# Kernel tuning notes

Measured on AMD Instinct MI355X. Metric: run time of the kernel, lower is better.

Reference implementation:

```python
import jax, jax.numpy as jnp
import numpy as np


def setup_inputs() -> dict:
    key = jax.random.key(0)
    k1, k2, k3 = jax.random.split(key, 3)
    B, H, S, D = 2, 8, 4096, 64
    queries = jax.random.normal(k1, (B, H, S, D), dtype=jnp.float32)
    keys = jax.random.normal(k2, (B, H, S, D), dtype=jnp.float32)
    values = jax.random.normal(k3, (B, H, S, D), dtype=jnp.float32)
    mask = jnp.zeros((1, 1, S, S), dtype=jnp.float32)
    return {"queries": queries, "keys": keys, "values": values, "d_k": D, "mask": mask}


def reference(queries, keys, values, d_k, mask):
    # scores: [B, H, Sq, Sk]
    scale = 1.0 / jnp.sqrt(jnp.asarray(d_k, dtype=queries.dtype))
    scores = jnp.einsum("bhqd,bhkd->bhqk", queries, keys) * scale
    scores = scores + (-1e9) * mask  # additive mask, broadcasts over B, H
    weights = jax.nn.softmax(scores, axis=-1)
    return jnp.einsum("bhqk,bhkd->bhqd", weights, values)
```

## Files before the change

kernel.cpp:

```cpp
#include <hip/hip_runtime.h>

#define S_LEN 4096
#define DHEAD 64
#define BQ    128
#define BK    64
#define NT    (S_LEN / BK)
#define KPAD  72

typedef __fp16   pk16x2 __attribute__((ext_vector_type(2)));
typedef _Float16 half4v __attribute__((ext_vector_type(4)));
typedef _Float16 half8  __attribute__((ext_vector_type(8)));
typedef float    f32x4  __attribute__((ext_vector_type(4)));

__global__ void mask_flag_kernel(const float4* __restrict__ mask, int* __restrict__ flag) {
    const long stride = 2048L * 256;
    long i = (long)blockIdx.x * 256 + threadIdx.x;
    int nz = 0;
    #pragma unroll
    for (int it = 0; it < 8; ++it) {
        float4 a = mask[i + it * stride];
        nz |= (a.x != 0.f) | (a.y != 0.f) | (a.z != 0.f) | (a.w != 0.f);
    }
    if (__any(nz)) {
        if ((threadIdx.x & 63) == 0) atomicOr(flag, 1);
    }
}

__global__ __launch_bounds__(256, 2) void attn_kernel(
    const float* __restrict__ Q, const float* __restrict__ K,
    const float* __restrict__ V, const int* __restrict__ dk,
    const float* __restrict__ mask, const int* __restrict__ maskflag,
    float* __restrict__ O)
{
    const int qt   = blockIdx.x;
    const int bh   = blockIdx.y;
    const int tid  = threadIdx.x;
    const int wave = tid >> 6;
    const int lane = tid & 63;
    const int l15  = lane & 15;
    const int quad = lane >> 4;

    const long base = (long)bh * S_LEN * DHEAD;
    const float* Qh = Q + base;
    const float* Kh = K + base;
    const float* Vh = V + base;
    float*       Oh = O + base;

    const int q0 = qt * BQ + wave * 32;
    const float csq  = rsqrtf((float)dk[0]) * 1.44269504088896f;
    const float mfac = -1e9f * 1.44269504088896f;
    const bool use_mask = (maskflag[0] != 0);

    __shared__ __align__(16) _Float16 Kt[2][BK][KPAD];
    __shared__ __align__(16) _Float16 Vt[2][DHEAD * KPAD];
    __shared__ __align__(16) _Float16 Pw[4][32][KPAD];

    half8 qf[2][2];
    #pragma unroll
    for (int f = 0; f < 2; ++f) {
        #pragma unroll
        for (int kc = 0; kc < 2; ++kc) {
            const float4* src = (const float4*)(Qh + (long)(q0 + f*16 + l15) * DHEAD + kc*32 + quad*8);
            float4 a = src[0], b = src[1];
            union { pk16x2 p[4]; half8 h; } u;
            u.p[0] = __builtin_amdgcn_cvt_pkrtz(a.x*csq, a.y*csq);
            u.p[1] = __builtin_amdgcn_cvt_pkrtz(a.z*csq, a.w*csq);
            u.p[2] = __builtin_amdgcn_cvt_pkrtz(b.x*csq, b.y*csq);
            u.p[3] = __builtin_amdgcn_cvt_pkrtz(b.z*csq, b.w*csq);
            qf[f][kc] = u.h;
        }
    }

    const int kr  = tid >> 2;
    const int ks  = tid & 3;
    const int vrp = tid >> 3;
    const int vdq = tid & 7;
    const float* Kb = Kh + (long)kr * DHEAD + ks * 16;
    const float* Vb = Vh + (long)(2 * vrp) * DHEAD + vdq * 8;
    const int vcol = (((vrp >> 2) ^ vdq) << 3) + ((2 * vrp) & 7);
    const int vd0  = vdq * 8;

    float4 kf[4], vf[4];
    auto load_tile = [&](int kt) {
        const float4* kp  = (const float4*)(Kb + (long)kt * BK * DHEAD);
        kf[0] = kp[0]; kf[1] = kp[1]; kf[2] = kp[2]; kf[3] = kp[3];
        const float4* vp0 = (const float4*)(Vb + (long)kt * BK * DHEAD);
        const float4* vp1 = (const float4*)(Vb + (long)kt * BK * DHEAD + DHEAD);
        vf[0] = vp0[0]; vf[1] = vp0[1]; vf[2] = vp1[0]; vf[3] = vp1[1];
    };
    auto store_tile = [&](int b) {
        union { pk16x2 p[4]; half8 h; } u0, u1;
        u0.p[0] = __builtin_amdgcn_cvt_pkrtz(kf[0].x, kf[0].y);
        u0.p[1] = __builtin_amdgcn_cvt_pkrtz(kf[0].z, kf[0].w);
        u0.p[2] = __builtin_amdgcn_cvt_pkrtz(kf[1].x, kf[1].y);
        u0.p[3] = __builtin_amdgcn_cvt_pkrtz(kf[1].z, kf[1].w);
        u1.p[0] = __builtin_amdgcn_cvt_pkrtz(kf[2].x, kf[2].y);
        u1.p[1] = __builtin_amdgcn_cvt_pkrtz(kf[2].z, kf[2].w);
        u1.p[2] = __builtin_amdgcn_cvt_pkrtz(kf[3].x, kf[3].y);
        u1.p[3] = __builtin_amdgcn_cvt_pkrtz(kf[3].z, kf[3].w);
        *(half8*)&Kt[b][kr][ks*16]     = u0.h;
        *(half8*)&Kt[b][kr][ks*16 + 8] = u1.h;
        _Float16* vt = &Vt[b][0];
        *(pk16x2*)&vt[(vd0+0)*KPAD + vcol] = __builtin_amdgcn_cvt_pkrtz(vf[0].x, vf[2].x);
        *(pk16x2*)&vt[(vd0+1)*KPAD + vcol] = __builtin_amdgcn_cvt_pkrtz(vf[0].y, vf[2].y);
        *(pk16x2*)&vt[(vd0+2)*KPAD + vcol] = __builtin_amdgcn_cvt_pkrtz(vf[0].z, vf[2].z);
        *(pk16x2*)&vt[(vd0+3)*KPAD + vcol] = __builtin_amdgcn_cvt_pkrtz(vf[0].w, vf[2].w);
        *(pk16x2*)&vt[(vd0+4)*KPAD + vcol] = __builtin_amdgcn_cvt_pkrtz(vf[1].x, vf[3].x);
        *(pk16x2*)&vt[(vd0+5)*KPAD + vcol] = __builtin_amdgcn_cvt_pkrtz(vf[1].y, vf[3].y);
        *(pk16x2*)&vt[(vd0+6)*KPAD + vcol] = __builtin_amdgcn_cvt_pkrtz(vf[1].z, vf[3].z);
        *(pk16x2*)&vt[(vd0+7)*KPAD + vcol] = __builtin_amdgcn_cvt_pkrtz(vf[1].w, vf[3].w);
    };

    f32x4 o[2][4];
    #pragma unroll
    for (int f = 0; f < 2; ++f)
        #pragma unroll
        for (int dt = 0; dt < 4; ++dt) o[f][dt] = (f32x4){0.f, 0.f, 0.f, 0.f};
    float m_i[2] = {-INFINITY, -INFINITY};
    float l_i[2] = {0.0f, 0.0f};

    load_tile(0);
    store_tile(0);
    __syncthreads();

    for (int kt = 0; kt < NT; ++kt) {
        const int b = kt & 1;
        if (kt + 1 < NT) load_tile(kt + 1);

        f32x4 st[2][4];
        #pragma unroll
        for (int f = 0; f < 2; ++f)
            #pragma unroll
            for (int nt = 0; nt < 4; ++nt) st[f][nt] = (f32x4){0.f,0.f,0.f,0.f};
        #pragma unroll
        for (int nt = 0; nt < 4; ++nt) {
            #pragma unroll
            for (int kc = 0; kc < 2; ++kc) {
                half8 af = *(const half8*)&Kt[b][nt*16 + l15][kc*32 + quad*8];
                st[0][nt] = __builtin_amdgcn_mfma_f32_16x16x32_f16(af, qf[0][kc], st[0][nt], 0, 0, 0);
                st[1][nt] = __builtin_amdgcn_mfma_f32_16x16x32_f16(af, qf[1][kc], st[1][nt], 0, 0, 0);
            }
        }

        if (use_mask) {
            #pragma unroll
            for (int f = 0; f < 2; ++f) {
                const long mrow = (long)(q0 + f*16 + l15) * S_LEN + kt*BK;
                #pragma unroll
                for (int nt = 0; nt < 4; ++nt)
                    #pragma unroll
                    for (int r = 0; r < 4; ++r)
                        st[f][nt][r] += mfac * mask[mrow + nt*16 + quad*4 + r];
            }
        }

        float alpha[2];
        #pragma unroll
        for (int f = 0; f < 2; ++f) {
            float mx = fmaxf(fmaxf(fmaxf(st[f][0][0], st[f][0][1]), fmaxf(st[f][0][2], st[f][0][3])),
                             fmaxf(fmaxf(st[f][1][0], st[f][1][1]), fmaxf(st[f][1][2], st[f][1][3])));
            float mx2 = fmaxf(fmaxf(fmaxf(st[f][2][0], st[f][2][1]), fmaxf(st[f][2][2], st[f][2][3])),
                              fmaxf(fmaxf(st[f][3][0], st[f][3][1]), fmaxf(st[f][3][2], st[f][3][3])));
            mx = fmaxf(mx, mx2);
            mx = fmaxf(mx, __shfl_xor(mx, 16, 64));
            mx = fmaxf(mx, __shfl_xor(mx, 32, 64));
            float mnew = fmaxf(m_i[f], mx);
            float rsum = 0.0f;
            #pragma unroll
            for (int nt = 0; nt < 4; ++nt) {
                #pragma unroll
                for (int r = 0; r < 4; ++r) {
                    float p = __builtin_amdgcn_exp2f(st[f][nt][r] - mnew);
                    st[f][nt][r] = p;
                    rsum += p;
                }
            }
            rsum += __shfl_xor(rsum, 16, 64);
            rsum += __shfl_xor(rsum, 32, 64);
            alpha[f] = __builtin_amdgcn_exp2f(m_i[f] - mnew);
            l_i[f] = alpha[f] * l_i[f] + rsum;
            m_i[f] = mnew;
        }

        #pragma unroll
        for (int f = 0; f < 2; ++f)
            #pragma unroll
            for (int r = 0; r < 4; ++r) {
                float a_r = __shfl(alpha[f], quad*4 + r, 64);
                #pragma unroll
                for (int dt = 0; dt < 4; ++dt) o[f][dt][r] *= a_r;
            }

        #pragma unroll
        for (int f = 0; f < 2; ++f)
            #pragma unroll
            for (int nt = 0; nt < 4; ++nt) {
                union { pk16x2 p[2]; half4v h; } up;
                up.p[0] = __builtin_amdgcn_cvt_pkrtz(st[f][nt][0], st[f][nt][1]);
                up.p[1] = __builtin_amdgcn_cvt_pkrtz(st[f][nt][2], st[f][nt][3]);
                *(half4v*)&Pw[wave][f*16 + l15][nt*16 + quad*4] = up.h;
            }

        #pragma unroll
        for (int kc2 = 0; kc2 < 2; ++kc2) {
            half8 pa0 = *(const half8*)&Pw[wave][l15][kc2*32 + quad*8];
            half8 pa1 = *(const half8*)&Pw[wave][16 + l15][kc2*32 + quad*8];
            #pragma unroll
            for (int dt = 0; dt < 4; ++dt) {
                const int row = dt*16 + l15;
                const int pb  = (4*kc2 + quad) ^ (row >> 3);
                half8 vb = *(const half8*)&Vt[b][row*KPAD + pb*8];
                o[0][dt] = __builtin_amdgcn_mfma_f32_16x16x32_f16(pa0, vb, o[0][dt], 0, 0, 0);
                o[1][dt] = __builtin_amdgcn_mfma_f32_16x16x32_f16(pa1, vb, o[1][dt], 0, 0, 0);
            }
        }

        if (kt + 1 < NT) {
            store_tile((kt + 1) & 1);
            __syncthreads();
        }
    }

    #pragma unroll
    for (int f = 0; f < 2; ++f) {
        #pragma unroll
        for (int r = 0; r < 4; ++r) {
            float lq = __shfl(l_i[f], quad*4 + r, 64);
            float linv = __builtin_amdgcn_rcpf(lq);
            const long row = (long)(q0 + f*16 + quad*4 + r) * DHEAD;
            #pragma unroll
            for (int dt = 0; dt < 4; ++dt)
                Oh[row + dt*16 + l15] = o[f][dt][r] * linv;
        }
    }
}

extern "C" void kernel_launch(void* const* d_in, const int* in_sizes, int n_in,
                              void* d_out, int out_size, void* d_ws, size_t ws_size,
                              hipStream_t stream) {
    const float* Q    = (const float*)d_in[0];
    const float* K    = (const float*)d_in[1];
    const float* V    = (const float*)d_in[2];
    const int*   dk   = (const int*)d_in[3];
    const float* mask = (const float*)d_in[4];
    float* out = (float*)d_out;
    int* flag = (int*)d_ws;

    (void)hipMemsetAsync(flag, 0, sizeof(int), stream);
    mask_flag_kernel<<<2048, 256, 0, stream>>>((const float4*)mask, flag);

    dim3 grid(S_LEN / BQ, 16);
    attn_kernel<<<grid, 256, 0, stream>>>(Q, K, V, dk, mask, flag, out);
}
```

Measured before the change: 255.5 us.

## Pre-convert K/V to swizzled fp16 tiles and stream them via global_load_lds

Adds a prepass kernel that converts K and V to fp16 once per call, transposing V and writing XOR-swizzled 64x64 tiles into workspace. The same kernel also folds in the mask nonzero scan. The attention kernel then double-buffers these tiles into LDS with direct global-to-LDS loads, which avoids per-block fp32 loads and conversions repeated across the 32 query tiles. The cost is an extra pass over K/V plus a workspace dependency, and the old path is kept as a fallback when the workspace is too small.

```diff
diff --git a/kernel.cpp b/kernel.cpp
--- a/kernel.cpp
+++ b/kernel.cpp
@@ -6,12 +6,21 @@
 #define BK    64
 #define NT    (S_LEN / BK)
 #define KPAD  72
+#define NBH   16
+#define TILE_HALFS (BK * DHEAD)
+#define WS_KV_HALFS ((size_t)NBH * NT * TILE_HALFS)
 
 typedef __fp16   pk16x2 __attribute__((ext_vector_type(2)));
 typedef _Float16 half4v __attribute__((ext_vector_type(4)));
 typedef _Float16 half8  __attribute__((ext_vector_type(8)));
 typedef float    f32x4  __attribute__((ext_vector_type(4)));
 
+__device__ __forceinline__ void gl_lds16(const _Float16* g, _Float16* l) {
+    __builtin_amdgcn_global_load_lds(
+        (const __attribute__((address_space(1))) unsigned int*)g,
+        (__attribute__((address_space(3))) unsigned int*)l, 16, 0, 0);
+}
+
 __global__ void mask_flag_kernel(const float4* __restrict__ mask, int* __restrict__ flag) {
     const long stride = 2048L * 256;
     long i = (long)blockIdx.x * 256 + threadIdx.x;
@@ -26,7 +35,252 @@
     }
 }
 
-__global__ __launch_bounds__(256, 2) void attn_kernel(
+__global__ void conv_kernel(const float* __restrict__ Kg, const float* __restrict__ Vg,
+                            const float* __restrict__ mask,
+                            _Float16* __restrict__ wsK, _Float16* __restrict__ wsV,
+                            int* __restrict__ flag) {
+    const int tid  = threadIdx.x;
+    const int tile = blockIdx.x;
+    __shared__ __align__(16) _Float16 T[64][64];
+
+    if (blockIdx.y == 0) {
+        const float* Ksrc = Kg + (long)tile * TILE_HALFS;
+        _Float16*    dst  = wsK + (long)tile * TILE_HALFS;
+        #pragma unroll
+        for (int it = 0; it < 2; ++it) {
+            int m = tid + it * 256;
+            int r = m >> 3, c = m & 7;
+            const float4* s4 = (const float4*)(Ksrc + r * DHEAD + ((c ^ (r & 7)) << 3));
+            float4 a = s4[0], b = s4[1];
+            union { pk16x2 p[4]; half8 h; } u;
+            u.p[0] = __builtin_amdgcn_cvt_pkrtz(a.x, a.y);
+            u.p[1] = __builtin_amdgcn_cvt_pkrtz(a.z, a.w);
+            u.p[2] = __builtin_amdgcn_cvt_pkrtz(b.x, b.y);
+            u.p[3] = __builtin_amdgcn_cvt_pkrtz(b.z, b.w);
+            *(half8*)(dst + m * 8) = u.h;
+        }
+    } else if (blockIdx.y == 1) {
+        const float* Vsrc = Vg + (long)tile * TILE_HALFS;
+        const int r  = tid >> 2;
+        const int d0 = (tid & 3) << 4;
+        const float4* s4 = (const float4*)(Vsrc + r * DHEAD + d0);
+        float vv[16];
+        *(float4*)&vv[0]  = s4[0];
+        *(float4*)&vv[4]  = s4[1];
+        *(float4*)&vv[8]  = s4[2];
+        *(float4*)&vv[12] = s4[3];
+        #pragma unroll
+        for (int j = 0; j < 16; j += 2) {
+            pk16x2 p = __builtin_amdgcn_cvt_pkrtz(vv[j], vv[j + 1]);
+            T[d0 + j][r]     = *((_Float16*)&p);
+            T[d0 + j + 1][r] = *((_Float16*)&p + 1);
+        }
+        __syncthreads();
+        _Float16* dst = wsV + (long)tile * TILE_HALFS;
+        #pragma unroll
+        for (int it = 0; it < 2; ++it) {
+            int m = tid + it * 256;
+            int d = m >> 3, c = m & 7;
+            *(half8*)(dst + m * 8) = *(const half8*)&T[d][(c ^ (d & 7)) << 3];
+        }
+    } else {
+        const float4* m4 = (const float4*)mask;
+        const long stride = 1024L * 256;
+        long i = (long)blockIdx.x * 256 + tid;
+        int nz = 0;
+        #pragma unroll
+        for (int it = 0; it < 16; ++it) {
+            float4 a = m4[i + it * stride];
+            nz |= (a.x != 0.f) | (a.y != 0.f) | (a.z != 0.f) | (a.w != 0.f);
+        }
+        if (__any(nz)) {
+            if ((tid & 63) == 0) atomicOr(flag, 1);
+        }
+    }
+}
+
+__global__ __launch_bounds__(256, 2) void attn_ws_kernel(
+    const float* __restrict__ Q, const _Float16* __restrict__ KW,
+    const _Float16* __restrict__ VW, const int* __restrict__ dk,
+    const float* __restrict__ mask, const int* __restrict__ maskflag,
+    float* __restrict__ O)
+{
+    const int qt   = blockIdx.x;
+    const int bh   = blockIdx.y;
+    const int tid  = threadIdx.x;
+    const int wave = tid >> 6;
+    const int lane = tid & 63;
+    const int l15  = lane & 15;
+    const int quad = lane >> 4;
+    const int sw   = (l15 & 7) << 3;
+    const int rq8  = quad << 3;
+
+    const long base = (long)bh * S_LEN * DHEAD;
+    const float* Qh = Q + base;
+    float*       Oh = O + base;
+    const _Float16* gk = KW + (long)bh * (NT * TILE_HALFS);
+    const _Float16* gv = VW + (long)bh * (NT * TILE_HALFS);
+
+    const int q0 = qt * BQ + wave * 32;
+    const float csq  = rsqrtf((float)dk[0]) * 1.44269504088896f;
+    const float mfac = -1e9f * 1.44269504088896f;
+    const bool use_mask = (maskflag[0] != 0);
+
+    __shared__ __align__(16) _Float16 KT[2][TILE_HALFS];
+    __shared__ __align__(16) _Float16 VT[2][TILE_HALFS];
+    __shared__ __align__(16) _Float16 Pw[4][32][KPAD];
+
+    half8 qf[2][2];
+    #pragma unroll
+    for (int f = 0; f < 2; ++f) {
+        #pragma unroll
+        for (int kc = 0; kc < 2; ++kc) {
+            const float4* src = (const float4*)(Qh + (long)(q0 + f*16 + l15) * DHEAD + kc*32 + rq8);
+            float4 a = src[0], b = src[1];
+            union { pk16x2 p[4]; half8 h; } u;
+            u.p[0] = __builtin_amdgcn_cvt_pkrtz(a.x*csq, a.y*csq);
+            u.p[1] = __builtin_amdgcn_cvt_pkrtz(a.z*csq, a.w*csq);
+            u.p[2] = __builtin_amdgcn_cvt_pkrtz(b.x*csq, b.y*csq);
+            u.p[3] = __builtin_amdgcn_cvt_pkrtz(b.z*csq, b.w*csq);
+            qf[f][kc] = u.h;
+        }
+    }
+
+    auto stage = [&](int kt, int b) {
+        const _Float16* k8 = gk + (long)kt * TILE_HALFS + tid * 8;
+        const _Float16* v8 = gv + (long)kt * TILE_HALFS + tid * 8;
+        gl_lds16(k8,        &KT[b][tid * 8]);
+        gl_lds16(k8 + 2048, &KT[b][2048 + tid * 8]);
+        gl_lds16(v8,        &VT[b][tid * 8]);
+        gl_lds16(v8 + 2048, &VT[b][2048 + tid * 8]);
+    };
+
+    f32x4 o[2][4];
+    #pragma unroll
+    for (int f = 0; f < 2; ++f)
+        #pragma unroll
+        for (int dt = 0; dt < 4; ++dt) o[f][dt] = (f32x4){0.f, 0.f, 0.f, 0.f};
+    float m_i[2] = {-INFINITY, -INFINITY};
+    float l_i[2] = {0.0f, 0.0f};
+
+    stage(0, 0);
+    __syncthreads();
+
+    for (int kt = 0; kt < NT; ++kt) {
+        const int b = kt & 1;
+        if (kt + 1 < NT) stage(kt + 1, b ^ 1);
+
+        f32x4 st[2][4];
+        #pragma unroll
+        for (int f = 0; f < 2; ++f)
+            #pragma unroll
+            for (int nt = 0; nt < 4; ++nt) st[f][nt] = (f32x4){0.f,0.f,0.f,0.f};
+        __builtin_amdgcn_s_setprio(1);
+        #pragma unroll
+        for (int nt = 0; nt < 4; ++nt) {
+            const int rb = (nt << 10) + (l15 << 6);
+            #pragma unroll
+            for (int kc = 0; kc < 2; ++kc) {
+                half8 af = *(const half8*)&KT[b][rb + ((kc*32 + rq8) ^ sw)];
+                st[0][nt] = __builtin_amdgcn_mfma_f32_16x16x32_f16(af, qf[0][kc], st[0][nt], 0, 0, 0);
+                st[1][nt] = __builtin_amdgcn_mfma_f32_16x16x32_f16(af, qf[1][kc], st[1][nt], 0, 0, 0);
+            }
+        }
+        __builtin_amdgcn_s_setprio(0);
+
+        if (use_mask) {
+            #pragma unroll
+            for (int f = 0; f < 2; ++f) {
+                const long mrow = (long)(q0 + f*16 + l15) * S_LEN + kt*BK;
+                #pragma unroll
+                for (int nt = 0; nt < 4; ++nt)
+                    #pragma unroll
+                    for (int r = 0; r < 4; ++r)
+                        st[f][nt][r] += mfac * mask[mrow + nt*16 + quad*4 + r];
+            }
+        }
+
+        #pragma unroll
+        for (int f = 0; f < 2; ++f) {
+            float mx = fmaxf(fmaxf(fmaxf(st[f][0][0], st[f][0][1]), fmaxf(st[f][0][2], st[f][0][3])),
+                             fmaxf(fmaxf(st[f][1][0], st[f][1][1]), fmaxf(st[f][1][2], st[f][1][3])));
+            float mx2 = fmaxf(fmaxf(fmaxf(st[f][2][0], st[f][2][1]), fmaxf(st[f][2][2], st[f][2][3])),
+                              fmaxf(fmaxf(st[f][3][0], st[f][3][1]), fmaxf(st[f][3][2], st[f][3][3])));
+            mx = fmaxf(mx, mx2);
+            mx = fmaxf(mx, __shfl_xor(mx, 16, 64));
+            mx = fmaxf(mx, __shfl_xor(mx, 32, 64));
+            const bool need = __any(mx > m_i[f]);
+            const float mnew = need ? fmaxf(m_i[f], mx) : m_i[f];
+            float rsum = 0.0f;
+            #pragma unroll
+            for (int nt = 0; nt < 4; ++nt) {
+                #pragma unroll
+                for (int r = 0; r < 4; ++r) {
+                    float p = __builtin_amdgcn_exp2f(st[f][nt][r] - mnew);
+                    st[f][nt][r] = p;
+                    rsum += p;
+                }
+            }
+            rsum += __shfl_xor(rsum, 16, 64);
+            rsum += __shfl_xor(rsum, 32, 64);
+            if (need) {
+                const float alpha = __builtin_amdgcn_exp2f(m_i[f] - mnew);
+                #pragma unroll
+                for (int r = 0; r < 4; ++r) {
+                    float a_r = __shfl(alpha, quad*4 + r, 64);
+                    #pragma unroll
+                    for (int dt = 0; dt < 4; ++dt) o[f][dt][r] *= a_r;
+                }
+                l_i[f] = alpha * l_i[f] + rsum;
+                m_i[f] = mnew;
+            } else {
+                l_i[f] += rsum;
+            }
+        }
+
+        #pragma unroll
+        for (int f = 0; f < 2; ++f)
+            #pragma unroll
+            for (int nt = 0; nt < 4; ++nt) {
+                union { pk16x2 p[2]; half4v h; } up;
+                up.p[0] = __builtin_amdgcn_cvt_pkrtz(st[f][nt][0], st[f][nt][1]);
+                up.p[1] = __builtin_amdgcn_cvt_pkrtz(st[f][nt][2], st[f][nt][3]);
+                *(half4v*)&Pw[wave][f*16 + l15][nt*16 + quad*4] = up.h;
+            }
+
+        __builtin_amdgcn_s_setprio(1);
+        #pragma unroll
+        for (int kc2 = 0; kc2 < 2; ++kc2) {
+            half8 pa0 = *(const half8*)&Pw[wave][l15][kc2*32 + rq8];
+            half8 pa1 = *(const half8*)&Pw[wave][16 + l15][kc2*32 + rq8];
+            #pragma unroll
+            for (int dt = 0; dt < 4; ++dt) {
+                const int db = (dt << 10) + (l15 << 6);
+                half8 vb = *(const half8*)&VT[b][db + ((kc2*32 + rq8) ^ sw)];
+                o[0][dt] = __builtin_amdgcn_mfma_f32_16x16x32_f16(pa0, vb, o[0][dt], 0, 0, 0);
+                o[1][dt] = __builtin_amdgcn_mfma_f32_16x16x32_f16(pa1, vb, o[1][dt], 0, 0, 0);
+            }
+        }
+        __builtin_amdgcn_s_setprio(0);
+
+        if (kt + 1 < NT) __syncthreads();
+    }
+
+    #pragma unroll
+    for (int f = 0; f < 2; ++f) {
+        #pragma unroll
+        for (int r = 0; r < 4; ++r) {
+            float lq = __shfl(l_i[f], quad*4 + r, 64);
+            float linv = __builtin_amdgcn_rcpf(lq);
+            const long row = (long)(q0 + f*16 + quad*4 + r) * DHEAD;
+            #pragma unroll
+            for (int dt = 0; dt < 4; ++dt)
+                Oh[row + dt*16 + l15] = o[f][dt][r] * linv;
+        }
+    }
+}
+
+__global__ __launch_bounds__(256, 2) void attn_kernel_fb(
     const float* __restrict__ Q, const float* __restrict__ K,
     const float* __restrict__ V, const int* __restrict__ dk,
     const float* __restrict__ mask, const int* __restrict__ maskflag,
@@ -247,8 +501,17 @@
     int* flag = (int*)d_ws;
 
     (void)hipMemsetAsync(flag, 0, sizeof(int), stream);
-    mask_flag_kernel<<<2048, 256, 0, stream>>>((const float4*)mask, flag);
-
-    dim3 grid(S_LEN / BQ, 16);
-    attn_kernel<<<grid, 256, 0, stream>>>(Q, K, V, dk, mask, flag, out);
+
+    const size_t WS_NEED = 256 + 2 * WS_KV_HALFS * sizeof(_Float16);
+    dim3 grid(S_LEN / BQ, NBH);
+
+    if (ws_size >= WS_NEED) {
+        _Float16* wsK = (_Float16*)((char*)d_ws + 256);
+        _Float16* wsV = wsK + WS_KV_HALFS;
+        conv_kernel<<<dim3(NBH * NT, 3), 256, 0, stream>>>(K, V, mask, wsK, wsV, flag);
+        attn_ws_kernel<<<grid, 256, 0, stream>>>(Q, wsK, wsV, dk, mask, flag, out);
+    } else {
+        mask_flag_kernel<<<2048, 256, 0, stream>>>((const float4*)mask, flag);
+        attn_kernel_fb<<<grid, 256, 0, stream>>>(Q, K, V, dk, mask, flag, out);
+    }
 }
```

New measurement: 275.4 us. 7.8% more time.

## Add lazy softmax rescaling, permlane32 swap reductions, and MFMA priority hints

Applied to the files above, without the earlier changes.

Skips the running-max update and the output accumulator rescale unless some row's new max exceeds the stored max by more than a threshold (8 in log2 units), checked wave-wide with __any. It also replaces the cross-32-lane shuffles in the max and sum reductions with permlane32_swap, and raises wave priority around both MFMA blocks with s_setprio. This cuts VALU and shuffle work in the softmax. In exchange, exponentials can reach up to 2^8 before rescaling, which adds fp16 overflow and precision risk in P.

```diff
diff --git a/kernel.cpp b/kernel.cpp
--- a/kernel.cpp
+++ b/kernel.cpp
@@ -11,6 +11,19 @@
 typedef _Float16 half4v __attribute__((ext_vector_type(4)));
 typedef _Float16 half8  __attribute__((ext_vector_type(8)));
 typedef float    f32x4  __attribute__((ext_vector_type(4)));
+typedef unsigned uint2v __attribute__((ext_vector_type(2)));
+
+__device__ __forceinline__ uint2v pls(unsigned x, unsigned y) {
+    return __builtin_amdgcn_permlane32_swap(x, y, false, false);
+}
+__device__ __forceinline__ float xmax32(float v) {
+    uint2v r = pls(__float_as_uint(v), __float_as_uint(v));
+    return fmaxf(__uint_as_float(r.x), __uint_as_float(r.y));
+}
+__device__ __forceinline__ float xadd32(float v) {
+    uint2v r = pls(__float_as_uint(v), __float_as_uint(v));
+    return __uint_as_float(r.x) + __uint_as_float(r.y);
+}
 
 __global__ void mask_flag_kernel(const float4* __restrict__ mask, int* __restrict__ flag) {
     const long stride = 2048L * 256;
@@ -132,6 +145,7 @@
         for (int f = 0; f < 2; ++f)
             #pragma unroll
             for (int nt = 0; nt < 4; ++nt) st[f][nt] = (f32x4){0.f,0.f,0.f,0.f};
+        __builtin_amdgcn_s_setprio(1);
         #pragma unroll
         for (int nt = 0; nt < 4; ++nt) {
             #pragma unroll
@@ -141,6 +155,7 @@
                 st[1][nt] = __builtin_amdgcn_mfma_f32_16x16x32_f16(af, qf[1][kc], st[1][nt], 0, 0, 0);
             }
         }
+        __builtin_amdgcn_s_setprio(0);
 
         if (use_mask) {
             #pragma unroll
@@ -154,7 +169,6 @@
             }
         }
 
-        float alpha[2];
         #pragma unroll
         for (int f = 0; f < 2; ++f) {
             float mx = fmaxf(fmaxf(fmaxf(st[f][0][0], st[f][0][1]), fmaxf(st[f][0][2], st[f][0][3])),
@@ -163,8 +177,9 @@
                               fmaxf(fmaxf(st[f][3][0], st[f][3][1]), fmaxf(st[f][3][2], st[f][3][3])));
             mx = fmaxf(mx, mx2);
             mx = fmaxf(mx, __shfl_xor(mx, 16, 64));
-            mx = fmaxf(mx, __shfl_xor(mx, 32, 64));
-            float mnew = fmaxf(m_i[f], mx);
+            mx = xmax32(mx);
+            const bool need = __any(mx > m_i[f] + 8.0f);
+            const float mnew = need ? fmaxf(m_i[f], mx) : m_i[f];
             float rsum = 0.0f;
             #pragma unroll
             for (int nt = 0; nt < 4; ++nt) {
@@ -176,20 +191,21 @@
                 }
             }
             rsum += __shfl_xor(rsum, 16, 64);
-            rsum += __shfl_xor(rsum, 32, 64);
-            alpha[f] = __builtin_amdgcn_exp2f(m_i[f] - mnew);
-            l_i[f] = alpha[f] * l_i[f] + rsum;
-            m_i[f] = mnew;
-        }
-
-        #pragma unroll
-        for (int f = 0; f < 2; ++f)
-            #pragma unroll
-            for (int r = 0; r < 4; ++r) {
-                float a_r = __shfl(alpha[f], quad*4 + r, 64);
+            rsum = xadd32(rsum);
+            if (need) {
+                const float alpha = __builtin_amdgcn_exp2f(m_i[f] - mnew);
                 #pragma unroll
-                for (int dt = 0; dt < 4; ++dt) o[f][dt][r] *= a_r;
-            }
+                for (int r = 0; r < 4; ++r) {
+                    float a_r = __shfl(alpha, quad*4 + r, 64);
+                    #pragma unroll
+                    for (int dt = 0; dt < 4; ++dt) o[f][dt][r] *= a_r;
+                }
+                l_i[f] = alpha * l_i[f] + rsum;
+                m_i[f] = mnew;
+            } else {
+                l_i[f] += rsum;
+            }
+        }
 
         #pragma unroll
         for (int f = 0; f < 2; ++f)
@@ -201,6 +217,7 @@
                 *(half4v*)&Pw[wave][f*16 + l15][nt*16 + quad*4] = up.h;
             }
 
+        __builtin_amdgcn_s_setprio(1);
         #pragma unroll
         for (int kc2 = 0; kc2 < 2; ++kc2) {
             half8 pa0 = *(const half8*)&Pw[wave][l15][kc2*32 + quad*8];
@@ -214,6 +231,7 @@
                 o[1][dt] = __builtin_amdgcn_mfma_f32_16x16x32_f16(pa1, vb, o[1][dt], 0, 0, 0);
             }
         }
+        __builtin_amdgcn_s_setprio(0);
 
         if (kt + 1 < NT) {
             store_tile((kt + 1) & 1);
```

Measured after the change: 248.4 us. -2.8%, faster.
